# Kernel tuning notes

Hardware: AMD Instinct MI355X
Metric: run time of the kernel (lower is better)

The kernel has to match this reference:

```python
import jax, jax.numpy as jnp
import numpy as np

N, L, D = 2, 2048, 1024
H, KV, HD = 16, 4, 64
CAP = 50.0


def _rope_cache(L, hd):
    inv_freq = 1.0 / (10000.0 ** (np.arange(0, hd, 2, dtype=np.float32) / hd))
    t = np.arange(L, dtype=np.float32)
    freqs = np.outer(t, inv_freq)                      # (L, hd/2)
    emb = np.concatenate([freqs, freqs], axis=-1)      # (L, hd)
    return jnp.asarray(np.cos(emb)), jnp.asarray(np.sin(emb))


def setup_inputs() -> dict:
    key = jax.random.key(0)
    ks = jax.random.split(key, 6)
    s = 0.02
    cos, sin = _rope_cache(L, HD)
    return {
        "x": jax.random.normal(ks[0], (N, L, D), jnp.float32),
        "Wq": jax.random.normal(ks[1], (D, H * HD), jnp.float32) * s,
        "bq": jnp.zeros((H * HD,), jnp.float32),
        "Wk": jax.random.normal(ks[2], (D, KV * HD), jnp.float32) * s,
        "bk": jnp.zeros((KV * HD,), jnp.float32),
        "Wv": jax.random.normal(ks[3], (D, KV * HD), jnp.float32) * s,
        "bv": jnp.zeros((KV * HD,), jnp.float32),
        "Wo": jax.random.normal(ks[4], (D, D), jnp.float32) * s,
        "bo": jnp.zeros((D,), jnp.float32),
        "q_gamma": jnp.ones((H, HD), jnp.float32),
        "k_gamma": jnp.ones((KV, HD), jnp.float32),
        "rope_cos": cos,
        "rope_sin": sin,
        "is_causal": 1,
    }


def _rmsnorm(t, gamma):
    # t: (N, heads, L, HD); gamma: (heads, HD)
    inv = jax.lax.rsqrt(jnp.mean(t * t, axis=-1, keepdims=True) + 1e-6)
    return t * inv * gamma[None, :, None, :]


def _apply_rope(t, cos, sin):
    # t: (N, heads, L, HD); cos/sin: (L, HD)
    hd = t.shape[-1]
    t1, t2 = t[..., : hd // 2], t[..., hd // 2:]
    rot = jnp.concatenate([-t2, t1], axis=-1)
    return t * cos[None, None] + rot * sin[None, None]


def reference(x, Wq, bq, Wk, bk, Wv, bv, Wo, bo, q_gamma, k_gamma, rope_cos, rope_sin, is_causal):
    n, l, d = x.shape
    h, hd = q_gamma.shape
    kv = k_gamma.shape[0]
    n_rep = h // kv

    q = (x @ Wq + bq).reshape(n, l, h, hd).transpose(0, 2, 1, 3)   # (n,h,l,hd)
    k = (x @ Wk + bk).reshape(n, l, kv, hd).transpose(0, 2, 1, 3)  # (n,kv,l,hd)
    v = (x @ Wv + bv).reshape(n, l, kv, hd).transpose(0, 2, 1, 3)

    q = _rmsnorm(q, q_gamma)
    k = _rmsnorm(k, k_gamma)
    q = _apply_rope(q, rope_cos, rope_sin)
    k = _apply_rope(k, rope_cos, rope_sin)

    if n_rep > 1:
        k = jnp.repeat(k, n_rep, axis=1)
        v = jnp.repeat(v, n_rep, axis=1)

    scale = hd ** -0.5
    logits = jnp.einsum("bhqd,bhkd->bhqk", q, k) * scale
    logits = CAP * jnp.tanh(logits / CAP)
    if is_causal:
        causal = jnp.tril(jnp.ones((l, l), dtype=bool))
        logits = jnp.where(causal[None, None], logits, -jnp.inf)
    weights = jax.nn.softmax(logits, axis=-1)
    y = jnp.einsum("bhqk,bhkd->bhqd", weights, v)
    y = y.transpose(0, 2, 1, 3).reshape(n, l, d)
    return y @ Wo + bo
```

## Files before the change

kernel.cpp:

```cpp
#include <hip/hip_runtime.h>
#include <hip/hip_bf16.h>

typedef __attribute__((ext_vector_type(8))) short short8;
typedef __attribute__((ext_vector_type(4))) float f32x4;
typedef __attribute__((ext_vector_type(4))) unsigned int u32x4;

using bf16 = __hip_bfloat16;

#define L_SEQ 2048
#define NB 2
#define DM 1024
#define NH 16
#define NKV 4
#define HDIM 64
#define CAPV 50.0f

#if __has_builtin(__builtin_amdgcn_exp2f)
#define EXP2(x) __builtin_amdgcn_exp2f(x)
#else
#define EXP2(x) exp2f(x)
#endif

__device__ __forceinline__ unsigned short f2bs(float f) {
  bf16 h = __float2bfloat16(f);
  return __builtin_bit_cast(unsigned short, h);
}

__device__ __forceinline__ float bs2f(unsigned short u) {
  return __bfloat162float(__builtin_bit_cast(bf16, u));
}

__device__ __forceinline__ unsigned int cvt_pk_bf16(float lo, float hi) {
  unsigned int w;
  asm("v_cvt_pk_bf16_f32 %0, %1, %2" : "=v"(w) : "v"(lo), "v"(hi));
  return w;
}

__device__ __forceinline__ void gload_lds16(const void* g, void* l) {
  __builtin_amdgcn_global_load_lds(
      (const __attribute__((address_space(1))) void*)g,
      (__attribute__((address_space(3))) void*)l, 16, 0, 0);
}

__global__ void k_cvt_x(const float* __restrict__ x, ushort* __restrict__ xb) {
  int i = (blockIdx.x * blockDim.x + threadIdx.x) * 4;
  float4 v = *reinterpret_cast<const float4*>(x + i);
  ushort4 o = make_ushort4(f2bs(v.x), f2bs(v.y), f2bs(v.z), f2bs(v.w));
  *reinterpret_cast<ushort4*>(xb + i) = o;
}

__global__ void k_transpose_all(const float* __restrict__ Wq, const float* __restrict__ Wk,
                                const float* __restrict__ Wv, const float* __restrict__ Wo,
                                bf16* __restrict__ wqt, bf16* __restrict__ wkt,
                                bf16* __restrict__ wvt, bf16* __restrict__ wot) {
  __shared__ float tile[32][33];
  const int z = blockIdx.z;
  const float* W = (z == 0) ? Wq : (z == 1) ? Wk : (z == 2) ? Wv : Wo;
  bf16* Wt = (z == 0) ? wqt : (z == 1) ? wkt : (z == 2) ? wvt : wot;
  const int Ncols = (z == 1 || z == 2) ? 256 : 1024;
  const int bx = blockIdx.x * 32;
  if (bx >= Ncols) return;
  const int by = blockIdx.y * 32;
  const int tx = threadIdx.x, ty = threadIdx.y;
  #pragma unroll
  for (int j = 0; j < 32; j += 8)
    tile[ty + j][tx] = W[(size_t)(by + ty + j) * Ncols + bx + tx];
  __syncthreads();
  #pragma unroll
  for (int j = 0; j < 32; j += 8)
    Wt[(size_t)(bx + ty + j) * 1024 + by + tx] = __float2bfloat16(tile[tx][ty + j]);
}

template<int OUT_MODE>
__global__ __launch_bounds__(256) void k_gemm(const bf16* __restrict__ A,
                                              const bf16* __restrict__ Bt,
                                              const float* __restrict__ bq,
                                              const float* __restrict__ bk,
                                              const float* __restrict__ bv,
                                              const float* __restrict__ qg,
                                              const float* __restrict__ kg,
                                              const float* __restrict__ rcT,
                                              const float* __restrict__ rsT,
                                              void* __restrict__ out0,
                                              void* __restrict__ out1,
                                              void* __restrict__ out2,
                                              const int* __restrict__ causal_flag,
                                              int M, int Ncols, int K) {
  __shared__ __align__(16) bf16 As[2][64 * 64];
  __shared__ __align__(16) bf16 Bs[2][128 * 64];
  const int t = threadIdx.x;
  const int lane = t & 63;
  const int w = t >> 6;
  const int wr = w >> 1, wc = w & 1;
  const int m0 = blockIdx.y * 64, n0 = blockIdx.x * 128;
  const int lr = lane & 15, lg = lane >> 4;
  const int nkt = K >> 6;

  bool heavy = false;
  const bf16* pO0 = nullptr;
  const bf16* pO1 = nullptr;
  const float* pdp = nullptr;
  if (OUT_MODE == 1) {
    heavy = ((*causal_flag) != 0) && ((m0 & 1024) != 0);
    pO0 = reinterpret_cast<const bf16*>(out1);
    pO1 = pO0 + (size_t)NB * L_SEQ * DM;
    pdp = reinterpret_cast<const float*>(out2);
  }

  f32x4 acc[2][4];
  #pragma unroll
  for (int m = 0; m < 2; ++m)
    #pragma unroll
    for (int n = 0; n < 4; ++n)
      acc[m][n] = f32x4{0.f, 0.f, 0.f, 0.f};

  short8 ra[2], rb[2];
  float rinv[2];
  auto issueA = [&](int kofs) {
    #pragma unroll
    for (int p = 0; p < 2; ++p) {
      const int G = p * 256 + w * 64 + lane;
      const int row = G >> 3, gc = G & 7;
      const int scol = kofs + ((gc ^ (row & 7)) * 8);
      const int grow = m0 + row;
      const int bb = grow >> 11, l = grow & 2047;
      const size_t base = ((size_t)bb * L_SEQ + l) * DM + scol;
      ra[p] = *reinterpret_cast<const short8*>(pO0 + base);
      rb[p] = *reinterpret_cast<const short8*>(pO1 + base);
      const int hh = scol >> 6;
      const float d0 = pdp[((size_t)bb * NH + hh) * L_SEQ + l];
      const float d1 = pdp[(size_t)(NB * NH) * L_SEQ + ((size_t)bb * NH + hh) * L_SEQ + l];
      rinv[p] = __builtin_amdgcn_rcpf(d0 + d1);
    }
  };
  auto writeA = [&](int buf) {
    #pragma unroll
    for (int p = 0; p < 2; ++p) {
      const int G = p * 256 + w * 64 + lane;
      const ushort* pa = reinterpret_cast<const ushort*>(&ra[p]);
      const ushort* pb = reinterpret_cast<const ushort*>(&rb[p]);
      unsigned int wo[4];
      #pragma unroll
      for (int i = 0; i < 4; ++i) {
        const float lo = (bs2f(pa[2 * i]) + bs2f(pb[2 * i])) * rinv[p];
        const float hi = (bs2f(pa[2 * i + 1]) + bs2f(pb[2 * i + 1])) * rinv[p];
        wo[i] = cvt_pk_bf16(lo, hi);
      }
      u32x4 pk = {wo[0], wo[1], wo[2], wo[3]};
      *reinterpret_cast<short8*>(&As[buf][G * 8]) = __builtin_bit_cast(short8, pk);
    }
  };
  auto gloadA = [&](int buf, int kofs) {
    #pragma unroll
    for (int p = 0; p < 2; ++p) {
      const int Gb = p * 256 + w * 64;
      const int G = Gb + lane;
      const int row = G >> 3, gc = G & 7;
      gload_lds16(&A[(size_t)(m0 + row) * K + kofs + ((gc ^ (row & 7)) * 8)],
                  &As[buf][Gb * 8]);
    }
  };
  auto gloadB = [&](int buf, int kofs) {
    #pragma unroll
    for (int p = 0; p < 4; ++p) {
      const int Gb = p * 256 + w * 64;
      const int G = Gb + lane;
      const int row = G >> 3, gc = G & 7;
      gload_lds16(&Bt[(size_t)(n0 + row) * K + kofs + ((gc ^ (row & 7)) * 8)],
                  &Bs[buf][Gb * 8]);
    }
  };
  auto mfmaStep = [&](int buf) {
    #pragma unroll
    for (int ks = 0; ks < 2; ++ks) {
      short8 af[2], bfr[4];
      #pragma unroll
      for (int m = 0; m < 2; ++m) {
        const int row = wr * 32 + m * 16 + lr;
        af[m] = *reinterpret_cast<const short8*>(
            &As[buf][row * 64 + (((ks * 4 + lg) ^ (row & 7)) * 8)]);
      }
      #pragma unroll
      for (int n = 0; n < 4; ++n) {
        const int row = wc * 64 + n * 16 + lr;
        bfr[n] = *reinterpret_cast<const short8*>(
            &Bs[buf][row * 64 + (((ks * 4 + lg) ^ (row & 7)) * 8)]);
      }
      #pragma unroll
      for (int m = 0; m < 2; ++m)
        #pragma unroll
        for (int n = 0; n < 4; ++n)
          acc[m][n] = __builtin_amdgcn_mfma_f32_16x16x32_bf16(af[m], bfr[n], acc[m][n], 0, 0, 0);
    }
  };

  int cur = 0;
  if (OUT_MODE == 1 && heavy) {
    issueA(0);
    writeA(0);
    gloadB(0, 0);
    for (int kt = 0; kt < nkt; ++kt) {
      __syncthreads();
      if (kt + 1 < nkt) {
        issueA((kt + 1) * 64);
        gloadB(cur ^ 1, (kt + 1) * 64);
      }
      mfmaStep(cur);
      if (kt + 1 < nkt) writeA(cur ^ 1);
      cur ^= 1;
    }
  } else {
    gloadA(0, 0);
    gloadB(0, 0);
    for (int kt = 0; kt < nkt; ++kt) {
      __syncthreads();
      if (kt + 1 < nkt) {
        gloadA(cur ^ 1, (kt + 1) * 64);
        gloadB(cur ^ 1, (kt + 1) * 64);
      }
      mfmaStep(cur);
      cur ^= 1;
    }
  }

  const int colbase = n0 + wc * 64;

  if (OUT_MODE == 1) {
    #pragma unroll
    for (int m = 0; m < 2; ++m) {
      const int row = m0 + wr * 32 + m * 16 + lg * 4;
      #pragma unroll
      for (int n = 0; n < 4; ++n) {
        const int col = colbase + n * 16 + lr;
        const float bvv = bq[col];
        #pragma unroll
        for (int r = 0; r < 4; ++r)
          reinterpret_cast<float*>(out0)[(size_t)(row + r) * Ncols + col] = acc[m][n][r] + bvv;
      }
    }
  } else {
    if (colbase >= 1280) {
      #pragma unroll
      for (int m = 0; m < 2; ++m) {
        const int row = m0 + wr * 32 + m * 16 + lg * 4;
        const int bb = row >> 11, l = row & 2047;
        #pragma unroll
        for (int n = 0; n < 4; ++n) {
          const int d = colbase - 1280 + n * 16 + lr;
          const float bvv = bv[d];
          ushort4 o;
          o.x = f2bs(acc[m][n][0] + bvv);
          o.y = f2bs(acc[m][n][1] + bvv);
          o.z = f2bs(acc[m][n][2] + bvv);
          o.w = f2bs(acc[m][n][3] + bvv);
          *reinterpret_cast<ushort4*>(
              &reinterpret_cast<bf16*>(out2)[((size_t)bb * 256 + d) * L_SEQ + l]) = o;
        }
      }
    } else {
      const bool isQ = (colbase < 1024);
      const float* bias = isQ ? bq : bk;
      const float* gma = isQ ? qg : kg;
      bf16* dst0 = reinterpret_cast<bf16*>(isQ ? out0 : out1);
      const int cb = isQ ? colbase : (colbase - 1024);
      const int head = cb >> 6;
      const int heads = isQ ? NH : NKV;
      float g[4];
      #pragma unroll
      for (int n = 0; n < 4; ++n) g[n] = gma[cb + n * 16 + lr];
      #pragma unroll
      for (int m = 0; m < 2; ++m) {
        const int row = m0 + wr * 32 + m * 16 + lg * 4;
        float vv[4][4];
        float ss[4] = {0.f, 0.f, 0.f, 0.f};
        #pragma unroll
        for (int n = 0; n < 4; ++n) {
          const float bvv = bias[cb + n * 16 + lr];
          #pragma unroll
          for (int r = 0; r < 4; ++r) {
            vv[n][r] = acc[m][n][r] + bvv;
            ss[r] = fmaf(vv[n][r], vv[n][r], ss[r]);
          }
        }
        #pragma unroll
        for (int r = 0; r < 4; ++r) {
          float s = ss[r];
          s += __shfl_xor(s, 1, 64);
          s += __shfl_xor(s, 2, 64);
          s += __shfl_xor(s, 4, 64);
          s += __shfl_xor(s, 8, 64);
          ss[r] = rsqrtf(s * (1.0f / 64.0f) + 1e-6f);
        }
        float tv[4][4];
        #pragma unroll
        for (int n = 0; n < 4; ++n)
          #pragma unroll
          for (int r = 0; r < 4; ++r)
            tv[n][r] = vv[n][r] * ss[r] * g[n];
        #pragma unroll
        for (int r = 0; r < 4; ++r) {
          const int grow = row + r;
          const int bb = grow >> 11, l = grow & 2047;
          bf16* dst = dst0 + (((size_t)bb * heads + head) * L_SEQ + l) * HDIM;
          #pragma unroll
          for (int n = 0; n < 4; ++n) {
            const int d = n * 16 + lr;
            const float c = rcT[l * HDIM + d];
            const float s2 = rsT[l * HDIM + d];
            const float rot = (n < 2) ? -tv[n ^ 2][r] : tv[n ^ 2][r];
            dst[d] = __float2bfloat16(fmaf(tv[n][r], c, rot * s2));
          }
        }
      }
    }
  }
}

__global__ __launch_bounds__(256) void k_attn(
    const bf16* __restrict__ qb, const bf16* __restrict__ kb,
    const bf16* __restrict__ vt, bf16* __restrict__ y,
    bf16* __restrict__ pO, float* __restrict__ pd,
    const int* __restrict__ causal_flag) {
  __shared__ __align__(16) bf16 Ks[2][64 * 64];
  __shared__ __align__(16) bf16 Vs[2][64 * 64];

  const int t = threadIdx.x, lane = t & 63, w = t >> 6;
  const int lr = lane & 15, lg = lane >> 4;
  const int jx = blockIdx.x;
  const int bh = blockIdx.y;
  const int half = blockIdx.z;
  const int b = bh >> 4, h = bh & 15;
  const int kvh = h >> 2;
  const bool causal = (*causal_flag) != 0;

  const int T_a = causal ? (2 * jx + 2) : 32;
  const int T_b = causal ? (32 - 2 * jx) : 32;
  const int total = T_a + T_b;
  const int mid = (total + 1) >> 1;
  const int g0 = half ? mid : 0;
  const int g1 = half ? total : mid;

  const bf16* kbase = kb + ((size_t)b * NKV + kvh) * L_SEQ * HDIM;
  const bf16* vbase = vt + ((size_t)b * NKV + kvh) * HDIM * L_SEQ;

  for (int seg = 0; seg < 2; ++seg) {
    const int qp = seg ? (15 - jx) : jx;
    const int ts = seg ? T_b : T_a;
    const int base = seg ? T_a : 0;
    const int lo = max(0, g0 - base);
    const int hi = min(ts, g1 - base);
    if (lo >= hi) continue;

    const int q0 = qp * 128;
    const int wrow = q0 + w * 32;

    short8 qf[2][2];
    #pragma unroll
    for (int s = 0; s < 2; ++s) {
      const bf16* qrow = qb + (((size_t)bh) * L_SEQ + wrow + s * 16 + lr) * HDIM;
      qf[s][0] = *reinterpret_cast<const short8*>(qrow + lg * 8);
      qf[s][1] = *reinterpret_cast<const short8*>(qrow + 32 + lg * 8);
    }

    f32x4 o0[4], o1[4];
    #pragma unroll
    for (int n = 0; n < 4; ++n) {
      o0[n] = f32x4{0.f, 0.f, 0.f, 0.f};
      o1[n] = f32x4{0.f, 0.f, 0.f, 0.f};
    }
    float plt0 = 0.f, plt1 = 0.f;

    __syncthreads();
    {
      const int k00 = lo * 64;
      #pragma unroll
      for (int i = 0; i < 2; ++i) {
        const int Gb = i * 256 + w * 64;
        const int G = Gb + lane;
        const int row = G >> 3, gc = G & 7;
        gload_lds16(kbase + (size_t)(k00 + row) * HDIM + ((gc ^ (row & 7)) * 8), &Ks[0][Gb * 8]);
        gload_lds16(vbase + (size_t)row * L_SEQ + k00 + ((gc ^ (row & 7)) * 8), &Vs[0][Gb * 8]);
      }
    }
    int cur = 0;

    for (int kt = lo; kt < hi; ++kt) {
      __syncthreads();

      if (kt + 1 < hi) {
        const int k0n = (kt + 1) * 64;
        #pragma unroll
        for (int i = 0; i < 2; ++i) {
          const int Gb = i * 256 + w * 64;
          const int G = Gb + lane;
          const int row = G >> 3, gc = G & 7;
          gload_lds16(kbase + (size_t)(k0n + row) * HDIM + ((gc ^ (row & 7)) * 8),
                      &Ks[cur ^ 1][Gb * 8]);
          gload_lds16(vbase + (size_t)row * L_SEQ + k0n + ((gc ^ (row & 7)) * 8),
                      &Vs[cur ^ 1][Gb * 8]);
        }
      }

      f32x4 s0[4], s1[4];
      #pragma unroll
      for (int n = 0; n < 4; ++n) {
        s0[n] = f32x4{0.f, 0.f, 0.f, 0.f};
        s1[n] = f32x4{0.f, 0.f, 0.f, 0.f};
      }
      #pragma unroll
      for (int n = 0; n < 4; ++n) {
        const int krow = n * 16 + lr;
        short8 kf0 = *reinterpret_cast<const short8*>(
            &Ks[cur][krow * 64 + ((lg ^ (krow & 7)) * 8)]);
        short8 kf1 = *reinterpret_cast<const short8*>(
            &Ks[cur][krow * 64 + (((4 + lg) ^ (krow & 7)) * 8)]);
        s0[n] = __builtin_amdgcn_mfma_f32_16x16x32_bf16(kf0, qf[0][0], s0[n], 0, 0, 0);
        s0[n] = __builtin_amdgcn_mfma_f32_16x16x32_bf16(kf1, qf[0][1], s0[n], 0, 0, 0);
        s1[n] = __builtin_amdgcn_mfma_f32_16x16x32_bf16(kf0, qf[1][0], s1[n], 0, 0, 0);
        s1[n] = __builtin_amdgcn_mfma_f32_16x16x32_bf16(kf1, qf[1][1], s1[n], 0, 0, 0);
      }

      const int k0 = kt * 64;
      #pragma unroll
      for (int n = 0; n < 4; ++n) {
        #pragma unroll
        for (int r = 0; r < 4; ++r) {
          float xs = s0[n][r];
          s0[n][r] = fmaf(xs * 0.18033688f, fmaf(xs * xs, -2.0833333e-6f, 1.0f), -16.0f);
          xs = s1[n][r];
          s1[n][r] = fmaf(xs * 0.18033688f, fmaf(xs * xs, -2.0833333e-6f, 1.0f), -16.0f);
        }
      }
      if (causal && (k0 + 63 > wrow)) {
        #pragma unroll
        for (int n = 0; n < 4; ++n) {
          const int keyb = k0 + n * 16 + lg * 4;
          #pragma unroll
          for (int r = 0; r < 4; ++r)
            if (keyb + r > wrow + lr) s0[n][r] = -1e30f;
        }
      }
      if (causal && (k0 + 63 > wrow + 16)) {
        #pragma unroll
        for (int n = 0; n < 4; ++n) {
          const int keyb = k0 + n * 16 + lg * 4;
          #pragma unroll
          for (int r = 0; r < 4; ++r)
            if (keyb + r > wrow + 16 + lr) s1[n][r] = -1e30f;
        }
      }

      unsigned int w0[8], w1[8];
      #pragma unroll
      for (int n = 0; n < 4; ++n) {
        const float a0 = EXP2(s0[n][0]);
        const float a1 = EXP2(s0[n][1]);
        const float a2 = EXP2(s0[n][2]);
        const float a3 = EXP2(s0[n][3]);
        plt0 += (a0 + a1) + (a2 + a3);
        w0[2 * n] = cvt_pk_bf16(a0, a1);
        w0[2 * n + 1] = cvt_pk_bf16(a2, a3);
        const float c0 = EXP2(s1[n][0]);
        const float c1 = EXP2(s1[n][1]);
        const float c2 = EXP2(s1[n][2]);
        const float c3 = EXP2(s1[n][3]);
        plt1 += (c0 + c1) + (c2 + c3);
        w1[2 * n] = cvt_pk_bf16(c0, c1);
        w1[2 * n + 1] = cvt_pk_bf16(c2, c3);
      }
      short8 pf0[2], pf1[2];
      #pragma unroll
      for (int ks = 0; ks < 2; ++ks) {
        u32x4 a = {w0[4 * ks], w0[4 * ks + 1], w0[4 * ks + 2], w0[4 * ks + 3]};
        u32x4 c = {w1[4 * ks], w1[4 * ks + 1], w1[4 * ks + 2], w1[4 * ks + 3]};
        pf0[ks] = __builtin_bit_cast(short8, a);
        pf1[ks] = __builtin_bit_cast(short8, c);
      }

      const int voff = 4 * (lg & 1);
      #pragma unroll
      for (int ks = 0; ks < 2; ++ks) {
        const int gA = 4 * ks + (lg >> 1);
        #pragma unroll
        for (int n = 0; n < 4; ++n) {
          const int vd = n * 16 + lr;
          const int vb_ = vd * 64;
          const int sw = vd & 7;
          const uint2 vlo = *reinterpret_cast<const uint2*>(
              &Vs[cur][vb_ + ((gA ^ sw) * 8 + voff)]);
          const uint2 vhi = *reinterpret_cast<const uint2*>(
              &Vs[cur][vb_ + (((gA + 2) ^ sw) * 8 + voff)]);
          u32x4 vv = {vlo.x, vlo.y, vhi.x, vhi.y};
          short8 vfr = __builtin_bit_cast(short8, vv);
          o0[n] = __builtin_amdgcn_mfma_f32_16x16x32_bf16(pf0[ks], vfr, o0[n], 0, 0, 0);
          o1[n] = __builtin_amdgcn_mfma_f32_16x16x32_bf16(pf1[ks], vfr, o1[n], 0, 0, 0);
        }
      }
      cur ^= 1;
    }

    const bool full = (lo == 0) && (hi == ts);
    #pragma unroll
    for (int s = 0; s < 2; ++s) {
      float ls = s ? plt1 : plt0;
      ls += __shfl_xor(ls, 16, 64);
      ls += __shfl_xor(ls, 32, 64);
      const f32x4* oa = s ? o1 : o0;
      if (full) {
        #pragma unroll
        for (int r = 0; r < 4; ++r) {
          const float den = __shfl(ls, lg * 4 + r, 64);
          const float invl = __builtin_amdgcn_rcpf(den);
          const int qg_ = wrow + s * 16 + lg * 4 + r;
          #pragma unroll
          for (int n = 0; n < 4; ++n)
            y[((size_t)b * L_SEQ + qg_) * DM + h * HDIM + n * 16 + lr] =
                __float2bfloat16(oa[n][r] * invl);
        }
      } else {
        if (lane < 16)
          pd[((size_t)half * NB * NH + bh) * L_SEQ + wrow + s * 16 + lane] = ls;
        #pragma unroll
        for (int r = 0; r < 4; ++r) {
          const int qg_ = wrow + s * 16 + lg * 4 + r;
          #pragma unroll
          for (int n = 0; n < 4; ++n)
            pO[(((size_t)half * NB + b) * L_SEQ + qg_) * DM + h * HDIM + n * 16 + lr] =
                __float2bfloat16(oa[n][r]);
        }
      }
    }
  }
}

extern "C" void kernel_launch(void* const* d_in, const int* in_sizes, int n_in,
                              void* d_out, int out_size, void* d_ws, size_t ws_size,
                              hipStream_t stream) {
  (void)in_sizes; (void)n_in; (void)out_size; (void)ws_size;
  const float* x  = (const float*)d_in[0];
  const float* Wq = (const float*)d_in[1];
  const float* bq = (const float*)d_in[2];
  const float* Wk = (const float*)d_in[3];
  const float* bk = (const float*)d_in[4];
  const float* Wv = (const float*)d_in[5];
  const float* bv = (const float*)d_in[6];
  const float* Wo = (const float*)d_in[7];
  const float* bo = (const float*)d_in[8];
  const float* qg = (const float*)d_in[9];
  const float* kg = (const float*)d_in[10];
  const float* rc = (const float*)d_in[11];
  const float* rs = (const float*)d_in[12];
  const int* causal = (const int*)d_in[13];
  float* out = (float*)d_out;

  char* ws = (char*)d_ws;
  size_t off = 0;
  auto alloc = [&](size_t bytes) -> char* {
    char* p = ws + off;
    off += (bytes + 255) & ~(size_t)255;
    return p;
  };
  bf16* xb    = (bf16*)alloc((size_t)4096 * 1024 * 2);
  bf16* wqkvt = (bf16*)alloc((size_t)1536 * 1024 * 2);
  bf16* wot   = (bf16*)alloc((size_t)1024 * 1024 * 2);
  bf16* vt    = (bf16*)alloc((size_t)NB * NKV * HDIM * L_SEQ * 2);
  bf16* qb    = (bf16*)alloc((size_t)NB * NH * L_SEQ * HDIM * 2);
  bf16* kb    = (bf16*)alloc((size_t)NB * NKV * L_SEQ * HDIM * 2);
  bf16* y     = (bf16*)alloc((size_t)4096 * 1024 * 2);
  bf16* pO    = (bf16*)alloc((size_t)2 * NB * L_SEQ * DM * 2);
  float* pd   = (float*)alloc((size_t)2 * NB * NH * L_SEQ * 4);
  bf16* wqt   = wqkvt;
  bf16* wkt   = wqkvt + (size_t)1024 * 1024;
  bf16* wvt   = wqkvt + (size_t)1280 * 1024;

  k_cvt_x<<<4096, 256, 0, stream>>>(x, (ushort*)xb);
  k_transpose_all<<<dim3(32, 32, 4), dim3(32, 8), 0, stream>>>(Wq, Wk, Wv, Wo, wqt, wkt, wvt, wot);

  k_gemm<6><<<dim3(12, 64), 256, 0, stream>>>(xb, wqkvt, bq, bk, bv, qg, kg, rc, rs,
                                              qb, kb, vt, causal, 4096, 1536, 1024);

  k_attn<<<dim3(8, NB * NH, 2), 256, 0, stream>>>(qb, kb, vt, y, pO, pd, causal);

  k_gemm<1><<<dim3(8, 64), 256, 0, stream>>>(y, wot, bo, nullptr, nullptr, nullptr, nullptr,
                                             nullptr, nullptr, out, pO, pd, causal,
                                             4096, 1024, 1024);
}
```

Baseline: 95.83 us.

## Fuse fp32-to-bf16 conversion of x into QKV GEMM and fold Q scale

Drops the separate x conversion kernel. The QKV GEMM now loads fp32 x straight into registers, packs it to bf16 and writes it into LDS, with the next tile's loads overlapped against the current MFMA step. It also folds the softmax scale into the Q rmsnorm gamma, which removes one multiply per logit in the attention tanh-approximation polynomial. The trade-off is that the GEMM reads twice as many A bytes and re-reads x across the 12 column blocks, and the A loads now go through registers instead of direct global-to-LDS loads.

After: 98.35 us. 1.03x slower.

```diff
diff --git a/kernel.cpp b/kernel.cpp
--- a/kernel.cpp
+++ b/kernel.cpp
@@ -14,6 +14,7 @@
 #define NKV 4
 #define HDIM 64
 #define CAPV 50.0f
+#define QSCALE 0.18033688f
 
 #if __has_builtin(__builtin_amdgcn_exp2f)
 #define EXP2(x) __builtin_amdgcn_exp2f(x)
@@ -40,13 +41,6 @@
   __builtin_amdgcn_global_load_lds(
       (const __attribute__((address_space(1))) void*)g,
       (__attribute__((address_space(3))) void*)l, 16, 0, 0);
-}
-
-__global__ void k_cvt_x(const float* __restrict__ x, ushort* __restrict__ xb) {
-  int i = (blockIdx.x * blockDim.x + threadIdx.x) * 4;
-  float4 v = *reinterpret_cast<const float4*>(x + i);
-  ushort4 o = make_ushort4(f2bs(v.x), f2bs(v.y), f2bs(v.z), f2bs(v.w));
-  *reinterpret_cast<ushort4*>(xb + i) = o;
 }
 
 __global__ void k_transpose_all(const float* __restrict__ Wq, const float* __restrict__ Wk,
@@ -72,7 +66,7 @@
 }
 
 template<int OUT_MODE>
-__global__ __launch_bounds__(256) void k_gemm(const bf16* __restrict__ A,
+__global__ __launch_bounds__(256) void k_gemm(const void* __restrict__ Ain,
                                               const bf16* __restrict__ Bt,
                                               const float* __restrict__ bq,
                                               const float* __restrict__ bk,
@@ -96,6 +90,9 @@
   const int lr = lane & 15, lg = lane >> 4;
   const int nkt = K >> 6;
 
+  const float* Af = reinterpret_cast<const float*>(Ain);
+  const bf16* Ab = reinterpret_cast<const bf16*>(Ain);
+
   bool heavy = false;
   const bf16* pO0 = nullptr;
   const bf16* pO1 = nullptr;
@@ -150,13 +147,34 @@
       *reinterpret_cast<short8*>(&As[buf][G * 8]) = __builtin_bit_cast(short8, pk);
     }
   };
+  float4 rf[2][2];
+  auto issueAx = [&](int kofs) {
+    #pragma unroll
+    for (int p = 0; p < 2; ++p) {
+      const int G = p * 256 + t;
+      const int row = G >> 3, gc = G & 7;
+      const int scol = kofs + ((gc ^ (row & 7)) * 8);
+      const float* src = Af + (size_t)(m0 + row) * K + scol;
+      rf[p][0] = *reinterpret_cast<const float4*>(src);
+      rf[p][1] = *reinterpret_cast<const float4*>(src + 4);
+    }
+  };
+  auto writeAx = [&](int buf) {
+    #pragma unroll
+    for (int p = 0; p < 2; ++p) {
+      const int G = p * 256 + t;
+      u32x4 pk = {cvt_pk_bf16(rf[p][0].x, rf[p][0].y), cvt_pk_bf16(rf[p][0].z, rf[p][0].w),
+                  cvt_pk_bf16(rf[p][1].x, rf[p][1].y), cvt_pk_bf16(rf[p][1].z, rf[p][1].w)};
+      *reinterpret_cast<short8*>(&As[buf][G * 8]) = __builtin_bit_cast(short8, pk);
+    }
+  };
   auto gloadA = [&](int buf, int kofs) {
     #pragma unroll
     for (int p = 0; p < 2; ++p) {
       const int Gb = p * 256 + w * 64;
       const int G = Gb + lane;
       const int row = G >> 3, gc = G & 7;
-      gload_lds16(&A[(size_t)(m0 + row) * K + kofs + ((gc ^ (row & 7)) * 8)],
+      gload_lds16(&Ab[(size_t)(m0 + row) * K + kofs + ((gc ^ (row & 7)) * 8)],
                   &As[buf][Gb * 8]);
     }
   };
@@ -195,7 +213,21 @@
   };
 
   int cur = 0;
-  if (OUT_MODE == 1 && heavy) {
+  if (OUT_MODE == 6) {
+    issueAx(0);
+    writeAx(0);
+    gloadB(0, 0);
+    for (int kt = 0; kt < nkt; ++kt) {
+      __syncthreads();
+      if (kt + 1 < nkt) {
+        issueAx((kt + 1) * 64);
+        gloadB(cur ^ 1, (kt + 1) * 64);
+      }
+      mfmaStep(cur);
+      if (kt + 1 < nkt) writeAx(cur ^ 1);
+      cur ^= 1;
+    }
+  } else if (OUT_MODE == 1 && heavy) {
     issueA(0);
     writeA(0);
     gloadB(0, 0);
@@ -265,9 +297,10 @@
       const int cb = isQ ? colbase : (colbase - 1024);
       const int head = cb >> 6;
       const int heads = isQ ? NH : NKV;
+      const float gsc = isQ ? QSCALE : 1.0f;
       float g[4];
       #pragma unroll
-      for (int n = 0; n < 4; ++n) g[n] = gma[cb + n * 16 + lr];
+      for (int n = 0; n < 4; ++n) g[n] = gma[cb + n * 16 + lr] * gsc;
       #pragma unroll
       for (int m = 0; m < 2; ++m) {
         const int row = m0 + wr * 32 + m * 16 + lg * 4;
@@ -426,9 +459,9 @@
         #pragma unroll
         for (int r = 0; r < 4; ++r) {
           float xs = s0[n][r];
-          s0[n][r] = fmaf(xs * 0.18033688f, fmaf(xs * xs, -2.0833333e-6f, 1.0f), -16.0f);
+          s0[n][r] = fmaf(xs, fmaf(xs * xs, -6.40607e-5f, 1.0f), -16.0f);
           xs = s1[n][r];
-          s1[n][r] = fmaf(xs * 0.18033688f, fmaf(xs * xs, -2.0833333e-6f, 1.0f), -16.0f);
+          s1[n][r] = fmaf(xs, fmaf(xs * xs, -6.40607e-5f, 1.0f), -16.0f);
         }
       }
       if (causal && (k0 + 63 > wrow)) {
@@ -560,7 +593,6 @@
     off += (bytes + 255) & ~(size_t)255;
     return p;
   };
-  bf16* xb    = (bf16*)alloc((size_t)4096 * 1024 * 2);
   bf16* wqkvt = (bf16*)alloc((size_t)1536 * 1024 * 2);
   bf16* wot   = (bf16*)alloc((size_t)1024 * 1024 * 2);
   bf16* vt    = (bf16*)alloc((size_t)NB * NKV * HDIM * L_SEQ * 2);
@@ -573,10 +605,9 @@
   bf16* wkt   = wqkvt + (size_t)1024 * 1024;
   bf16* wvt   = wqkvt + (size_t)1280 * 1024;
 
-  k_cvt_x<<<4096, 256, 0, stream>>>(x, (ushort*)xb);
   k_transpose_all<<<dim3(32, 32, 4), dim3(32, 8), 0, stream>>>(Wq, Wk, Wv, Wo, wqt, wkt, wvt, wot);
 
-  k_gemm<6><<<dim3(12, 64), 256, 0, stream>>>(xb, wqkvt, bq, bk, bv, qg, kg, rc, rs,
+  k_gemm<6><<<dim3(12, 64), 256, 0, stream>>>(x, wqkvt, bq, bk, bv, qg, kg, rc, rs,
                                               qb, kb, vt, causal, 4096, 1536, 1024);
 
   k_attn<<<dim3(8, NB * NH, 2), 256, 0, stream>>>(qb, kb, vt, y, pO, pd, causal);
```
